# Kernel tuning notes

Measured on AMD Instinct MI355X. Metric: run time of the kernel, lower is better.

The kernel has to match this reference:

```python
import jax, jax.numpy as jnp
import numpy as np

B, S, C, H = 2, 3144, 256, 8
HD = C // H                      # head_dim = key_dim = 32
SCALE = HD ** -0.5
QN = 8                           # queriesNum hard-coded in source
KS = 5                           # lepe depthwise conv kernel


def setup_inputs() -> dict:
    key = jax.random.key(0)
    ks = jax.random.split(key, 10)
    gain_qkv = 2 ** (-2.5) * (2.0 / (C + C)) ** 0.5  # xavier_normal std with gain 2^-2.5
    gain_out = (2.0 / (C + C)) ** 0.5
    return {
        "x": jax.random.normal(ks[0], (B, S, C), jnp.float32),
        "mask": jax.random.uniform(ks[1], (B, S, S), jnp.float32),
        "wq": jax.random.normal(ks[2], (C, C), jnp.float32) * gain_qkv,
        "bq": jnp.zeros((C,), jnp.float32),
        "wk": jax.random.normal(ks[3], (C, C), jnp.float32) * gain_qkv,
        "bk": jnp.zeros((C,), jnp.float32),
        "wv": jax.random.normal(ks[4], (C, C), jnp.float32) * gain_qkv,
        "bv": jnp.zeros((C,), jnp.float32),
        "lepe_w": jax.random.normal(ks[5], (KS, KS, 1, C), jnp.float32) * 0.05,  # depthwise HWIO
        "lepe_b": jnp.zeros((C,), jnp.float32),
        "wo": jax.random.normal(ks[6], (C, C), jnp.float32) * gain_out,
        "bo": jnp.zeros((C,), jnp.float32),
        "h": 56,
        "w": 56,
    }


def _dwconv(x_nhwc, kern, bias):
    # depthwise 5x5, stride 1, padding 2 (groups = channels)
    y = jax.lax.conv_general_dilated(
        x_nhwc, kern, window_strides=(1, 1), padding=((2, 2), (2, 2)),
        dimension_numbers=("NHWC", "HWIO", "NHWC"),
        feature_group_count=x_nhwc.shape[-1])
    return y + bias


def reference(x, mask, wq, bq, wk, bk, wv, bv, lepe_w, lepe_b, wo, bo, h, w):
    b, s, c = x.shape
    q = x @ wq.T + bq
    k = (x @ wk.T + bk) * SCALE
    v = x @ wv.T + bv
    # lepe positional residual on the non-query tokens
    lepe = _dwconv(v[:, QN:].reshape(b, h, w, c), lepe_w, lepe_b).reshape(b, h * w, c)
    qh = q.reshape(b, s, H, HD).transpose(0, 2, 1, 3)   # (b, H, s, hd)
    kh = k.reshape(b, s, H, HD).transpose(0, 2, 1, 3)
    vh = kh  # faithful to source: v_h = k.reshape(...)  (scaled k used as values)
    qk = jnp.einsum("bhqd,bhkd->bhqk", qh, kh)
    qk = qk + jnp.log(mask[:, None] + 1e-6)              # isSoftMask=True path
    attn = jax.nn.softmax(qk, axis=-1)
    out = jnp.einsum("bhqk,bhkd->bhqd", attn, vh)
    out = out.transpose(0, 2, 1, 3).reshape(b, s, c)
    out = out.at[:, QN:].add(lepe)
    return out @ wo.T + bo
```

## Files before the change

kernel.cpp:

```cpp
#include <hip/hip_runtime.h>


#define S_LEN 3144
#define SP    3200
#define HEADS 8
#define HD    32
#define BATCH 2
#define MROWS (BATCH*S_LEN)
#define NPIX  3136
#define SCALE_F 0.17677669529663687f

typedef __bf16 bf16x8  __attribute__((ext_vector_type(8)));
typedef __bf16 bf16x4  __attribute__((ext_vector_type(4)));
typedef float  floatx4 __attribute__((ext_vector_type(4)));
typedef short  shortx4 __attribute__((ext_vector_type(4)));

static __device__ __forceinline__ float bf2f(unsigned int h) {
  union { unsigned int u; float f; } v; v.u = h << 16; return v.f;
}
static __device__ __forceinline__ unsigned short f2bf(float f) {
  union { __bf16 b; unsigned short u; } v; v.b = (__bf16)f; return v.u;
}
static __device__ __forceinline__ bf16x8 ldcvt8(const float* __restrict__ p) {
  float4 a = *(const float4*)p;
  float4 b = *(const float4*)(p + 4);
  bf16x8 r;
  r[0]=(__bf16)a.x; r[1]=(__bf16)a.y; r[2]=(__bf16)a.z; r[3]=(__bf16)a.w;
  r[4]=(__bf16)b.x; r[5]=(__bf16)b.y; r[6]=(__bf16)b.z; r[7]=(__bf16)b.w;
  return r;
}

#define GLOBAL_AS __attribute__((address_space(1)))
#define LDS_AS    __attribute__((address_space(3)))
static __device__ __forceinline__ void gload_lds16(const void* g, void* l) {
  __builtin_amdgcn_global_load_lds((const GLOBAL_AS void*)g, (LDS_AS void*)l, 16, 0, 0);
}

__global__ __launch_bounds__(256) void k_qkv(
    const float* __restrict__ x,
    const float* __restrict__ wqp, const float* __restrict__ bqp,
    const float* __restrict__ wkp, const float* __restrict__ bkp,
    const float* __restrict__ wvp, const float* __restrict__ bvp,
    unsigned short* __restrict__ qws, unsigned short* __restrict__ kws,
    unsigned short* __restrict__ vfrag, unsigned short* __restrict__ vstage)
{
  __shared__ unsigned short lds_t[64 * 65];
  const int lane = threadIdx.x & 63;
  const int wid  = threadIdx.x >> 6;
  const int c    = lane & 15, quad = lane >> 4;
  const int bsel  = blockIdx.x / 50;
  const int stile = blockIdx.x % 50;
  const int srow0 = stile * 64;
  const int ncol = blockIdx.y * 64;
  const int wsel = ncol >> 8;
  const int col0 = ncol & 255;

  const float* wptr = (wsel == 0) ? wqp : (wsel == 1) ? wkp : wvp;
  const float* bptr = (wsel == 0) ? bqp : (wsel == 1) ? bkp : bvp;

  const int srow = srow0 + wid * 16 + c;
  const int arow = bsel * S_LEN + ((srow < S_LEN) ? srow : 0);
  const float* ap = x    + (size_t)arow * 256 + quad * 8;
  const float* bp = wptr + (size_t)(col0 + c) * 256 + quad * 8;

  floatx4 acc[4];
#pragma unroll
  for (int ct = 0; ct < 4; ++ct) acc[ct] = (floatx4){0.f, 0.f, 0.f, 0.f};

#pragma unroll
  for (int ks = 0; ks < 8; ++ks) {
    bf16x8 af = ldcvt8(ap + ks * 32);
#pragma unroll
    for (int ct = 0; ct < 4; ++ct) {
      bf16x8 bf = ldcvt8(bp + (size_t)ct * 16 * 256 + ks * 32);
      acc[ct] = __builtin_amdgcn_mfma_f32_16x16x32_bf16(af, bf, acc[ct], 0, 0, 0);
    }
  }

#pragma unroll
  for (int ct = 0; ct < 4; ++ct) {
    const int col = col0 + ct * 16 + c;
    const float bias = bptr[col];
#pragma unroll
    for (int r = 0; r < 4; ++r) {
      const int s = srow0 + quad * 4 + r + wid * 16;
      const int valid = (s < S_LEN);
      const float v = acc[ct][r] + bias;
      if (wsel == 0) {
        qws[(((size_t)(bsel * HEADS + (col >> 5))) * SP + s) * HD + (col & 31)] =
            valid ? f2bf(v) : (unsigned short)0;
      } else if (wsel == 1) {
        const unsigned short kb16 = valid ? f2bf(v * SCALE_F) : (unsigned short)0;
        kws[(((size_t)(bsel * HEADS + (col >> 5))) * SP + s) * HD + (col & 31)] = kb16;
        lds_t[(ct * 16 + c) * 65 + (wid * 16 + quad * 4 + r)] = kb16;
      } else {
        if (valid) vstage[(size_t)(bsel * S_LEN + s) * 256 + col] = f2bf(v);
      }
    }
  }

  if (wsel == 1) {
    __syncthreads();
    const int tid = threadIdx.x;
#pragma unroll
    for (int j = 0; j < 4; ++j) {
      const int grp  = j * 4 + (tid >> 6);
      const int l    = tid & 63;
      const int ct2  = grp & 3;
      const int half = (grp >> 2) & 1;
      const int hsel = grp >> 3;
      const int cc = l & 15, qq = l >> 4;
      const int cl = hsel * 32 + half * 16 + cc;
      const int rb = ct2 * 16 + qq * 4;
      union { shortx4 s4; unsigned short u[4]; } pk;
#pragma unroll
      for (int e = 0; e < 4; ++e) pk.u[e] = lds_t[cl * 65 + rb + e];
      const int hglob = (col0 >> 5) + hsel;
      const size_t off =
          ((((size_t)(bsel * HEADS + hglob) * 50 + stile) * 4 + ct2) * 2 + half) * 64 + l;
      *(shortx4*)(vfrag + off * 4) = pk.s4;
    }
  }
}

__global__ __launch_bounds__(256) void k_lepe(const unsigned short* __restrict__ vws,
                                              const float* __restrict__ cw,
                                              const float* __restrict__ cb,
                                              unsigned short* __restrict__ lepe)
{
  int idx = blockIdx.x * 256 + threadIdx.x;
  if (idx >= BATCH * NPIX * 32) return;
  const int cg = idx & 31;
  const int p  = (idx >> 5) % NPIX;
  const int b  = idx / (NPIX * 32);
  const int y  = p / 56, xx = p - y * 56;

  float acc[8];
  {
    float4 b0 = *(const float4*)(cb + cg * 8);
    float4 b1 = *(const float4*)(cb + cg * 8 + 4);
    acc[0]=b0.x; acc[1]=b0.y; acc[2]=b0.z; acc[3]=b0.w;
    acc[4]=b1.x; acc[5]=b1.y; acc[6]=b1.z; acc[7]=b1.w;
  }
#pragma unroll
  for (int dy = -2; dy <= 2; ++dy) {
    const int yy = y + dy;
    if ((unsigned)yy >= 56u) continue;
#pragma unroll
    for (int dx = -2; dx <= 2; ++dx) {
      const int xs = xx + dx;
      if ((unsigned)xs >= 56u) continue;
      uint4 vv = *(const uint4*)(vws + (size_t)(b * S_LEN + 8 + yy * 56 + xs) * 256 + cg * 8);
      const float* wp = cw + (size_t)((dy + 2) * 5 + (dx + 2)) * 256 + cg * 8;
      float4 w0 = *(const float4*)wp;
      float4 w1 = *(const float4*)(wp + 4);
      unsigned int va[4] = {vv.x, vv.y, vv.z, vv.w};
      acc[0] += bf2f(va[0] & 0xFFFFu) * w0.x;  acc[1] += bf2f(va[0] >> 16) * w0.y;
      acc[2] += bf2f(va[1] & 0xFFFFu) * w0.z;  acc[3] += bf2f(va[1] >> 16) * w0.w;
      acc[4] += bf2f(va[2] & 0xFFFFu) * w1.x;  acc[5] += bf2f(va[2] >> 16) * w1.y;
      acc[6] += bf2f(va[3] & 0xFFFFu) * w1.z;  acc[7] += bf2f(va[3] >> 16) * w1.w;
    }
  }
  unsigned int o[4];
#pragma unroll
  for (int j = 0; j < 4; ++j)
    o[j] = (unsigned int)f2bf(acc[2*j]) | ((unsigned int)f2bf(acc[2*j+1]) << 16);
  *((uint4*)(lepe + (size_t)(b * NPIX + p) * 256 + cg * 8)) = make_uint4(o[0], o[1], o[2], o[3]);
}

template<bool TAIL>
static __device__ __forceinline__ void proc_tile(
    int t, const unsigned short* __restrict__ kb,
    const unsigned short* __restrict__ vb,
    const float* __restrict__ mb,
    int c, int quad, int lane, const bf16x8 qf,
    floatx4& o0, floatx4& o1, float& l_run)
{
  const int k0 = t * 64;
  bf16x8 kf[4]; shortx4 v0[4], v1[4];
  const unsigned short* tb = vb + (size_t)t * 2048;
#pragma unroll
  for (int ct = 0; ct < 4; ++ct) {
    kf[ct] = *(const bf16x8*)(kb + (size_t)(k0 + ct * 16 + c) * HD + quad * 8);
    v0[ct] = *(const shortx4*)(tb + (ct * 2 + 0) * 256 + lane * 4);
    v1[ct] = *(const shortx4*)(tb + (ct * 2 + 1) * 256 + lane * 4);
  }
  floatx4 s[4];
#pragma unroll
  for (int ct = 0; ct < 4; ++ct)
    s[ct] = __builtin_amdgcn_mfma_f32_16x16x32_bf16(kf[ct], qf,
               (floatx4){0.f,0.f,0.f,0.f}, 0, 0, 0);
  float ls = 0.f;
  shortx4 pf[4];
#pragma unroll
  for (int ct = 0; ct < 4; ++ct) {
    const float4 mv = *(const float4*)(mb + c * 64 + (((ct * 4 + quad) ^ c) * 4));
    float pr[4];
    pr[0] = (mv.x + 1e-6f) * __expf(s[ct][0]);
    pr[1] = (mv.y + 1e-6f) * __expf(s[ct][1]);
    pr[2] = (mv.z + 1e-6f) * __expf(s[ct][2]);
    pr[3] = (mv.w + 1e-6f) * __expf(s[ct][3]);
    if (TAIL) {
      const int kk = k0 + ct * 16 + quad * 4;
#pragma unroll
      for (int r = 0; r < 4; ++r) if (kk + r >= S_LEN) pr[r] = 0.f;
    }
    ls += (pr[0] + pr[1]) + (pr[2] + pr[3]);
    union { bf16x4 b4; shortx4 s4; } u;
    u.b4[0]=(__bf16)pr[0]; u.b4[1]=(__bf16)pr[1]; u.b4[2]=(__bf16)pr[2]; u.b4[3]=(__bf16)pr[3];
    pf[ct] = u.s4;
  }
  l_run += ls;
#pragma unroll
  for (int ct = 0; ct < 4; ++ct) {
    o0 = __builtin_amdgcn_mfma_f32_16x16x16bf16_1k(v0[ct], pf[ct], o0, 0, 0, 0);
    o1 = __builtin_amdgcn_mfma_f32_16x16x16bf16_1k(v1[ct], pf[ct], o1, 0, 0, 0);
  }
}

__global__ __launch_bounds__(256) void k_flash(
    const unsigned short* __restrict__ qws,
    const unsigned short* __restrict__ kws,
    const unsigned short* __restrict__ vfrag,
    const float* __restrict__ mask,
    const unsigned short* __restrict__ lepe,
    unsigned short* __restrict__ attn)
{
  __shared__ __align__(16) float smem[4][2048];
  const int lane = threadIdx.x & 63;
  const int wid  = threadIdx.x >> 6;
  const int c    = lane & 15, quad = lane >> 4;
  const int u    = blockIdx.x;
  const int xcd  = u & 7;
  const int slot = u >> 3;
  const int h    = slot & 7;
  const int p    = (slot >> 3) * 8 + xcd;
  const int b    = p / 200;
  const int strip = p - b * 200;
  const int qrow = strip * 16 + c;
  const size_t bh = (size_t)(b * HEADS + h);

  const bf16x8 qf = *(const bf16x8*)(qws + (bh * SP + qrow) * HD + quad * 8);
  const unsigned short* kb = kws + bh * SP * HD;
  const unsigned short* vb = vfrag + bh * (size_t)(50 * 2048);
  float* mt = &smem[wid][0];

  const float* msrc[4];
  int goff4[4];
#pragma unroll
  for (int i = 0; i < 4; ++i) {
    const int rq = i * 4 + (lane >> 4);
    int mr = strip * 16 + rq; if (mr >= S_LEN) mr = S_LEN - 1;
    msrc[i] = mask + ((size_t)b * S_LEN + mr) * S_LEN;
    goff4[i] = ((lane & 15) ^ rq) * 4;
  }

  float l_run = 0.f;
  floatx4 o0 = (floatx4){0.f,0.f,0.f,0.f};
  floatx4 o1 = (floatx4){0.f,0.f,0.f,0.f};

  const int nt = (wid < 2) ? 13 : 12;

  {
    const int k0 = (wid * 12) * 64;
#pragma unroll
    for (int i = 0; i < 4; ++i)
      gload_lds16(msrc[i] + (k0 + goff4[i]), mt + i * 256);
  }

  for (int it = 0; it < nt; ++it) {
    const int t = (it < 12) ? wid * 12 + it : 48 + wid;
    if (it + 1 < nt) {
      const int tn = (it + 1 < 12) ? wid * 12 + it + 1 : 48 + wid;
      const int k0n = tn * 64;
      float* dst = mt + ((it + 1) & 1) * 1024;
      const bool tailn = (k0n + 63 >= S_LEN);
#pragma unroll
      for (int i = 0; i < 4; ++i) {
        int kk = k0n + goff4[i];
        if (tailn && kk > S_LEN - 4) kk = S_LEN - 4;
        gload_lds16(msrc[i] + kk, dst + i * 256);
      }
      asm volatile("s_waitcnt vmcnt(4)" ::: "memory");
    } else {
      asm volatile("s_waitcnt vmcnt(0)" ::: "memory");
    }
    const float* mb = mt + (it & 1) * 1024;
    if (wid == 1 && it == 12)
      proc_tile<true >(t, kb, vb, mb, c, quad, lane, qf, o0, o1, l_run);
    else
      proc_tile<false>(t, kb, vb, mb, c, quad, lane, qf, o0, o1, l_run);
  }

#pragma unroll
  for (int r = 0; r < 4; ++r) {
    smem[wid][lane * 9 + r]     = o0[r];
    smem[wid][lane * 9 + 4 + r] = o1[r];
  }
  smem[wid][lane * 9 + 8] = l_run;
  __syncthreads();

  if (wid == 0) {
#pragma unroll
    for (int w = 1; w < 4; ++w) {
#pragma unroll
      for (int r = 0; r < 4; ++r) {
        o0[r] += smem[w][lane * 9 + r];
        o1[r] += smem[w][lane * 9 + 4 + r];
      }
      l_run += smem[w][lane * 9 + 8];
    }
    l_run += __shfl_xor(l_run, 16);
    l_run += __shfl_xor(l_run, 32);
    const float rl = 1.f / l_run;

    if (qrow < S_LEN) {
      const size_t obase = ((size_t)b * S_LEN + qrow) * 256 + h * 32;
      const size_t lbase = (qrow >= 8) ? (((size_t)b * NPIX + (qrow - 8)) * 256 + h * 32) : 0;
#pragma unroll
      for (int mt2 = 0; mt2 < 2; ++mt2) {
        floatx4 ov = mt2 ? o1 : o0;
#pragma unroll
        for (int r = 0; r < 4; ++r) {
          const int d = mt2 * 16 + quad * 4 + r;
          float val = ov[r] * rl;
          if (qrow >= 8) val += bf2f(lepe[lbase + d]);
          attn[obase + d] = f2bf(val);
        }
      }
    }
  }
}

__global__ __launch_bounds__(256) void k_oproj(
    const unsigned short* __restrict__ attn,
    const float* __restrict__ wop,
    const float* __restrict__ bop,
    float* __restrict__ out)
{
  const int lane = threadIdx.x & 63;
  const int wid  = threadIdx.x >> 6;
  const int c = lane & 15, quad = lane >> 4;
  const int row0 = blockIdx.x * 64 + wid * 16;
  const int col0 = blockIdx.y * 64;

  int arow = row0 + c; if (arow >= MROWS) arow = 0;
  const unsigned short* ap = attn + (size_t)arow * 256 + quad * 8;
  const float* bp = wop + (size_t)(col0 + c) * 256 + quad * 8;

  floatx4 acc[4];
#pragma unroll
  for (int ct = 0; ct < 4; ++ct) acc[ct] = (floatx4){0.f,0.f,0.f,0.f};
#pragma unroll
  for (int ks = 0; ks < 8; ++ks) {
    bf16x8 af = *(const bf16x8*)(ap + ks * 32);
#pragma unroll
    for (int ct = 0; ct < 4; ++ct) {
      bf16x8 bf = ldcvt8(bp + (size_t)ct * 16 * 256 + ks * 32);
      acc[ct] = __builtin_amdgcn_mfma_f32_16x16x32_bf16(af, bf, acc[ct], 0, 0, 0);
    }
  }
#pragma unroll
  for (int ct = 0; ct < 4; ++ct) {
    const int col = col0 + ct * 16 + c;
    const float bias = bop[col];
#pragma unroll
    for (int r = 0; r < 4; ++r) {
      const int row = row0 + quad * 4 + r;
      if (row >= MROWS) continue;
      out[(size_t)row * 256 + col] = acc[ct][r] + bias;
    }
  }
}

#define QW_OFF 0u
#define KW_OFF 3276800u
#define VF_OFF 6553600u
#define LE_OFF 9830400u
#define AT_OFF 13041664u

extern "C" void kernel_launch(void* const* d_in, const int* in_sizes, int n_in,
                              void* d_out, int out_size, void* d_ws, size_t ws_size,
                              hipStream_t stream) {
  const float* x    = (const float*)d_in[0];
  const float* mask = (const float*)d_in[1];
  const float* wq   = (const float*)d_in[2];
  const float* bq   = (const float*)d_in[3];
  const float* wk   = (const float*)d_in[4];
  const float* bk   = (const float*)d_in[5];
  const float* wv   = (const float*)d_in[6];
  const float* bv   = (const float*)d_in[7];
  const float* lw   = (const float*)d_in[8];
  const float* lb   = (const float*)d_in[9];
  const float* wo   = (const float*)d_in[10];
  const float* bo   = (const float*)d_in[11];

  char* ws = (char*)d_ws;
  unsigned short* qws = (unsigned short*)(ws + QW_OFF);
  unsigned short* kws = (unsigned short*)(ws + KW_OFF);
  unsigned short* vfr = (unsigned short*)(ws + VF_OFF);
  unsigned short* lpe = (unsigned short*)(ws + LE_OFF);
  unsigned short* atb = (unsigned short*)(ws + AT_OFF);
  unsigned short* vst = (unsigned short*)d_out;
  float*          outf = (float*)d_out;

  k_qkv<<<dim3(100, 12), 256, 0, stream>>>(x, wq, bq, wk, bk, wv, bv, qws, kws, vfr, vst);
  k_lepe<<<784, 256, 0, stream>>>(vst, lw, lb, lpe);
  k_flash<<<3200, 256, 0, stream>>>(qws, kws, vfr, mask, lpe, atb);
  k_oproj<<<dim3(99, 4), 256, 0, stream>>>(atb, wo, bo, outf);
}
```

Baseline: 324.5 us.

## Pre-convert QKV inputs to bf16, use exp2 softmax, split flash keys across 8 waves

Adds a conversion kernel that turns x and the QKV weights into bf16 in scratch buffers, so the projection GEMM loads bf16 directly instead of converting fp32 on every load. K is stored pre-multiplied by scale*log2(e) so the softmax can use the hardware exp2 instruction. The flash kernel moves from 4 to 8 waves per block, halving each wave's key-tile count and doubling the cross-wave reduction. Risks are the extra launch and traffic, doubled LDS per block lowering occupancy, and the new xb staging region in d_out that vstage and k_lepe still use.

```diff
diff --git a/kernel.cpp b/kernel.cpp
--- a/kernel.cpp
+++ b/kernel.cpp
@@ -9,6 +9,7 @@
 #define MROWS (BATCH*S_LEN)
 #define NPIX  3136
 #define SCALE_F 0.17677669529663687f
+#define KQ_SC   0.25504472665352026f
 
 typedef __bf16 bf16x8  __attribute__((ext_vector_type(8)));
 typedef __bf16 bf16x4  __attribute__((ext_vector_type(4)));
@@ -36,11 +37,36 @@
   __builtin_amdgcn_global_load_lds((const GLOBAL_AS void*)g, (LDS_AS void*)l, 16, 0, 0);
 }
 
+#define FENCE4() asm volatile("s_waitcnt vmcnt(4)" ::: "memory")
+#define FENCE0() asm volatile("s_waitcnt vmcnt(0)" ::: "memory")
+
+__global__ __launch_bounds__(256) void k_cvt(
+    const float* __restrict__ x, const float* __restrict__ wq,
+    const float* __restrict__ wk, const float* __restrict__ wv,
+    unsigned short* __restrict__ xb, unsigned short* __restrict__ w3b)
+{
+  const int i = blockIdx.x * 256 + threadIdx.x;
+  const int NX = MROWS * 32;
+  const int NW = 8192;
+  const float* src;
+  unsigned short* dst;
+  if (i < NX) { src = x + (size_t)i * 8; dst = xb + (size_t)i * 8; }
+  else {
+    const int j = i - NX;
+    if (j >= 3 * NW) return;
+    src = (j < NW) ? wq + (size_t)j * 8
+        : (j < 2 * NW) ? wk + (size_t)(j - NW) * 8
+                       : wv + (size_t)(j - 2 * NW) * 8;
+    dst = w3b + (size_t)j * 8;
+  }
+  bf16x8 v = ldcvt8(src);
+  *(bf16x8*)dst = v;
+}
+
 __global__ __launch_bounds__(256) void k_qkv(
-    const float* __restrict__ x,
-    const float* __restrict__ wqp, const float* __restrict__ bqp,
-    const float* __restrict__ wkp, const float* __restrict__ bkp,
-    const float* __restrict__ wvp, const float* __restrict__ bvp,
+    const unsigned short* __restrict__ xb, const unsigned short* __restrict__ w3b,
+    const float* __restrict__ bqp, const float* __restrict__ bkp,
+    const float* __restrict__ bvp,
     unsigned short* __restrict__ qws, unsigned short* __restrict__ kws,
     unsigned short* __restrict__ vfrag, unsigned short* __restrict__ vstage)
 {
@@ -55,13 +81,12 @@
   const int wsel = ncol >> 8;
   const int col0 = ncol & 255;
 
-  const float* wptr = (wsel == 0) ? wqp : (wsel == 1) ? wkp : wvp;
   const float* bptr = (wsel == 0) ? bqp : (wsel == 1) ? bkp : bvp;
 
   const int srow = srow0 + wid * 16 + c;
   const int arow = bsel * S_LEN + ((srow < S_LEN) ? srow : 0);
-  const float* ap = x    + (size_t)arow * 256 + quad * 8;
-  const float* bp = wptr + (size_t)(col0 + c) * 256 + quad * 8;
+  const unsigned short* ap = xb  + (size_t)arow * 256 + quad * 8;
+  const unsigned short* bp = w3b + (size_t)(ncol + c) * 256 + quad * 8;
 
   floatx4 acc[4];
 #pragma unroll
@@ -69,10 +94,10 @@
 
 #pragma unroll
   for (int ks = 0; ks < 8; ++ks) {
-    bf16x8 af = ldcvt8(ap + ks * 32);
+    bf16x8 af = *(const bf16x8*)(ap + ks * 32);
 #pragma unroll
     for (int ct = 0; ct < 4; ++ct) {
-      bf16x8 bf = ldcvt8(bp + (size_t)ct * 16 * 256 + ks * 32);
+      bf16x8 bf = *(const bf16x8*)(bp + (size_t)ct * 16 * 256 + ks * 32);
       acc[ct] = __builtin_amdgcn_mfma_f32_16x16x32_bf16(af, bf, acc[ct], 0, 0, 0);
     }
   }
@@ -83,16 +108,17 @@
     const float bias = bptr[col];
 #pragma unroll
     for (int r = 0; r < 4; ++r) {
-      const int s = srow0 + quad * 4 + r + wid * 16;
+      const int s = srow0 + wid * 16 + quad * 4 + r;
       const int valid = (s < S_LEN);
       const float v = acc[ct][r] + bias;
       if (wsel == 0) {
         qws[(((size_t)(bsel * HEADS + (col >> 5))) * SP + s) * HD + (col & 31)] =
             valid ? f2bf(v) : (unsigned short)0;
       } else if (wsel == 1) {
-        const unsigned short kb16 = valid ? f2bf(v * SCALE_F) : (unsigned short)0;
-        kws[(((size_t)(bsel * HEADS + (col >> 5))) * SP + s) * HD + (col & 31)] = kb16;
-        lds_t[(ct * 16 + c) * 65 + (wid * 16 + quad * 4 + r)] = kb16;
+        kws[(((size_t)(bsel * HEADS + (col >> 5))) * SP + s) * HD + (col & 31)] =
+            valid ? f2bf(v * KQ_SC) : (unsigned short)0;
+        lds_t[(ct * 16 + c) * 65 + (wid * 16 + quad * 4 + r)] =
+            valid ? f2bf(v * SCALE_F) : (unsigned short)0;
       } else {
         if (valid) vstage[(size_t)(bsel * S_LEN + s) * 256 + col] = f2bf(v);
       }
@@ -196,10 +222,10 @@
   for (int ct = 0; ct < 4; ++ct) {
     const float4 mv = *(const float4*)(mb + c * 64 + (((ct * 4 + quad) ^ c) * 4));
     float pr[4];
-    pr[0] = (mv.x + 1e-6f) * __expf(s[ct][0]);
-    pr[1] = (mv.y + 1e-6f) * __expf(s[ct][1]);
-    pr[2] = (mv.z + 1e-6f) * __expf(s[ct][2]);
-    pr[3] = (mv.w + 1e-6f) * __expf(s[ct][3]);
+    pr[0] = (mv.x + 1e-6f) * __builtin_amdgcn_exp2f(s[ct][0]);
+    pr[1] = (mv.y + 1e-6f) * __builtin_amdgcn_exp2f(s[ct][1]);
+    pr[2] = (mv.z + 1e-6f) * __builtin_amdgcn_exp2f(s[ct][2]);
+    pr[3] = (mv.w + 1e-6f) * __builtin_amdgcn_exp2f(s[ct][3]);
     if (TAIL) {
       const int kk = k0 + ct * 16 + quad * 4;
 #pragma unroll
@@ -218,7 +244,26 @@
   }
 }
 
-__global__ __launch_bounds__(256) void k_flash(
+static __device__ __forceinline__ void stage_mask(
+    const float* const (&msrc)[4], const int (&goff4)[4], int k0, float* dst)
+{
+#pragma unroll
+  for (int i = 0; i < 4; ++i)
+    gload_lds16(msrc[i] + (k0 + goff4[i]), dst + i * 256);
+}
+
+static __device__ __forceinline__ void stage_mask_tail(
+    const float* const (&msrc)[4], const int (&goff4)[4], int k0, float* dst)
+{
+#pragma unroll
+  for (int i = 0; i < 4; ++i) {
+    int kk = k0 + goff4[i];
+    if (kk > S_LEN - 4) kk = S_LEN - 4;
+    gload_lds16(msrc[i] + kk, dst + i * 256);
+  }
+}
+
+__global__ __launch_bounds__(512) void k_flash(
     const unsigned short* __restrict__ qws,
     const unsigned short* __restrict__ kws,
     const unsigned short* __restrict__ vfrag,
@@ -226,7 +271,7 @@
     const unsigned short* __restrict__ lepe,
     unsigned short* __restrict__ attn)
 {
-  __shared__ __align__(16) float smem[4][2048];
+  __shared__ __align__(16) float smem[8][2048];
   const int lane = threadIdx.x & 63;
   const int wid  = threadIdx.x >> 6;
   const int c    = lane & 15, quad = lane >> 4;
@@ -259,34 +304,24 @@
   floatx4 o0 = (floatx4){0.f,0.f,0.f,0.f};
   floatx4 o1 = (floatx4){0.f,0.f,0.f,0.f};
 
-  const int nt = (wid < 2) ? 13 : 12;
-
-  {
-    const int k0 = (wid * 12) * 64;
-#pragma unroll
-    for (int i = 0; i < 4; ++i)
-      gload_lds16(msrc[i] + (k0 + goff4[i]), mt + i * 256);
-  }
+  const int tbase = wid * 6;
+  const int nt = (wid < 2) ? 7 : 6;
+
+  stage_mask(msrc, goff4, tbase * 64, mt);
 
   for (int it = 0; it < nt; ++it) {
-    const int t = (it < 12) ? wid * 12 + it : 48 + wid;
+    const int t = (it < 6) ? tbase + it : 48 + wid;
     if (it + 1 < nt) {
-      const int tn = (it + 1 < 12) ? wid * 12 + it + 1 : 48 + wid;
-      const int k0n = tn * 64;
+      const int tn = (it + 1 < 6) ? tbase + it + 1 : 48 + wid;
       float* dst = mt + ((it + 1) & 1) * 1024;
-      const bool tailn = (k0n + 63 >= S_LEN);
-#pragma unroll
-      for (int i = 0; i < 4; ++i) {
-        int kk = k0n + goff4[i];
-        if (tailn && kk > S_LEN - 4) kk = S_LEN - 4;
-        gload_lds16(msrc[i] + kk, dst + i * 256);
-      }
-      asm volatile("s_waitcnt vmcnt(4)" ::: "memory");
+      if (tn == 49) stage_mask_tail(msrc, goff4, 49 * 64, dst);
+      else          stage_mask(msrc, goff4, tn * 64, dst);
+      FENCE4();
     } else {
-      asm volatile("s_waitcnt vmcnt(0)" ::: "memory");
+      FENCE0();
     }
     const float* mb = mt + (it & 1) * 1024;
-    if (wid == 1 && it == 12)
+    if (wid == 1 && it == 6)
       proc_tile<true >(t, kb, vb, mb, c, quad, lane, qf, o0, o1, l_run);
     else
       proc_tile<false>(t, kb, vb, mb, c, quad, lane, qf, o0, o1, l_run);
@@ -302,7 +337,7 @@
 
   if (wid == 0) {
 #pragma unroll
-    for (int w = 1; w < 4; ++w) {
+    for (int w = 1; w < 8; ++w) {
 #pragma unroll
       for (int r = 0; r < 4; ++r) {
         o0[r] += smem[w][lane * 9 + r];
@@ -399,13 +434,16 @@
   unsigned short* qws = (unsigned short*)(ws + QW_OFF);
   unsigned short* kws = (unsigned short*)(ws + KW_OFF);
   unsigned short* vfr = (unsigned short*)(ws + VF_OFF);
+  unsigned short* w3b = (unsigned short*)(ws + LE_OFF);
   unsigned short* lpe = (unsigned short*)(ws + LE_OFF);
   unsigned short* atb = (unsigned short*)(ws + AT_OFF);
   unsigned short* vst = (unsigned short*)d_out;
+  unsigned short* xb  = (unsigned short*)d_out + 1609728;
   float*          outf = (float*)d_out;
 
-  k_qkv<<<dim3(100, 12), 256, 0, stream>>>(x, wq, bq, wk, bk, wv, bv, qws, kws, vfr, vst);
+  k_cvt<<<882, 256, 0, stream>>>(x, wq, wk, wv, xb, w3b);
+  k_qkv<<<dim3(100, 12), 256, 0, stream>>>(xb, w3b, bq, bk, bv, qws, kws, vfr, vst);
   k_lepe<<<784, 256, 0, stream>>>(vst, lw, lb, lpe);
-  k_flash<<<3200, 256, 0, stream>>>(qws, kws, vfr, mask, lpe, atb);
+  k_flash<<<3200, 512, 0, stream>>>(qws, kws, vfr, mask, lpe, atb);
   k_oproj<<<dim3(99, 4), 256, 0, stream>>>(atb, wo, bo, outf);
 }
```

After: 311.8 us. 3.9% less time.
